# Optimization experiments

Hardware: AMD Instinct MI355X
Metric: run time of the kernel (lower is better)

## Reference

```python
import jax, jax.numpy as jnp
import numpy as np

BN_EPS = 1e-5

def _conv1x1(w, b, x):
    # w: (O, C), b: (O,), x: (B, C, T) -> (B, O, T)
    return jnp.einsum('oc,bct->bot', w, x) + b[None, :, None]

def _maxpool2(x):
    # MaxPool1d(kernel_size=2, stride=2): (B, C, T) -> (B, C, T//2)
    B, C, T = x.shape
    return x.reshape(B, C, T // 2, 2).max(axis=-1)

def setup_inputs() -> dict:
    key = jax.random.key(0)
    ks = jax.random.split(key, 11)
    B, C, Ci, T = 4, 256, 128, 8192
    s_in = 1.0 / np.sqrt(C)
    s_ic = 1.0 / np.sqrt(Ci)
    return {
        'x':       jax.random.normal(ks[0], (B, C, T), dtype=jnp.float32),
        'theta_w': jax.random.uniform(ks[1], (Ci, C), jnp.float32, -s_in, s_in),
        'theta_b': jax.random.uniform(ks[2], (Ci,),   jnp.float32, -s_in, s_in),
        'phi_w':   jax.random.uniform(ks[3], (Ci, C), jnp.float32, -s_in, s_in),
        'phi_b':   jax.random.uniform(ks[4], (Ci,),   jnp.float32, -s_in, s_in),
        'g_w':     jax.random.uniform(ks[5], (Ci, C), jnp.float32, -s_in, s_in),
        'g_b':     jax.random.uniform(ks[6], (Ci,),   jnp.float32, -s_in, s_in),
        'w_w':     jax.random.uniform(ks[7], (C, Ci), jnp.float32, -s_ic, s_ic),
        'w_b':     jax.random.uniform(ks[8], (C,),    jnp.float32, -s_ic, s_ic),
        'gamma':   jax.random.normal(ks[9], (C,), dtype=jnp.float32),
        'beta':    jax.random.normal(ks[10], (C,), dtype=jnp.float32),
    }

def reference(x, theta_w, theta_b, phi_w, phi_b, g_w, g_b, w_w, w_b, gamma, beta):
    # x: (B, C, T)
    theta = _conv1x1(theta_w, theta_b, x)            # (B, Ci, T)
    phi   = _maxpool2(_conv1x1(phi_w, phi_b, x))     # (B, Ci, N), N = T//2
    g     = _maxpool2(_conv1x1(g_w, g_b, x))         # (B, Ci, N)
    N = phi.shape[-1]
    # f = theta^T phi / N  (dot-product similarity, divide-by-N normalization)
    f = jnp.einsum('bct,bcn->btn', theta, phi) / N   # (B, T, N)
    y = jnp.einsum('btn,bcn->bct', f, g)             # (B, Ci, T)
    wy = _conv1x1(w_w, w_b, y)                       # (B, C, T)
    # BatchNorm1d (training mode: batch statistics over (B, T), biased var)
    mean = wy.mean(axis=(0, 2), keepdims=True)
    var = ((wy - mean) ** 2).mean(axis=(0, 2), keepdims=True)
    bn = gamma[None, :, None] * (wy - mean) * jax.lax.rsqrt(var + BN_EPS) + beta[None, :, None]
    return bn + x
```

## Files before the change

### kernel.cpp

```cpp
#include <hip/hip_runtime.h>
#include <hip/hip_bf16.h>


constexpr int B = 4, C = 256, CI = 128, T = 8192, NN = 4096;

using s16x8 = __attribute__((ext_vector_type(8))) short;
using f32x4 = __attribute__((ext_vector_type(4))) float;

__device__ __forceinline__ unsigned short f2bf(float f) {
    unsigned int x = __float_as_uint(f);
    unsigned int r = (x + 0x7fffu + ((x >> 16) & 1u)) >> 16;
    return (unsigned short)r;
}
__device__ __forceinline__ float bf2f(unsigned short u) {
    return __uint_as_float((unsigned int)u << 16);
}

#define MFMA(a, b, c) __builtin_amdgcn_mfma_f32_16x16x32_bf16((a), (b), (c), 0, 0, 0)

__device__ __forceinline__ void glds16(const unsigned short* g, void* l) {
    __builtin_amdgcn_global_load_lds(
        (const __attribute__((address_space(1))) unsigned int*)(g),
        (__attribute__((address_space(3))) unsigned int*)(l), 16, 0, 0);
}


constexpr size_t SZ_XT = (size_t)B * T * C * 2;
constexpr size_t O_XTH = 0;
constexpr size_t O_XTL = O_XTH + SZ_XT;
constexpr size_t O_WSH = O_XTL + SZ_XT;
constexpr size_t O_WSL = O_WSH + (size_t)C * C * 2;
constexpr size_t SZ_P  = (size_t)B * CI * NN * 2;
constexpr size_t O_PH  = O_WSL + (size_t)C * C * 2;
constexpr size_t O_PL  = O_PH + SZ_P;
constexpr size_t O_GH  = O_PL + SZ_P;
constexpr size_t O_GL  = O_GH + SZ_P;
constexpr size_t O_WY  = O_PH;
constexpr size_t O_S   = O_GL + SZ_P;
constexpr size_t O_M   = O_S  + (size_t)B * CI * CI * 4;
constexpr size_t O_W2H = O_M  + (size_t)B * C * CI * 4;
constexpr size_t O_W2L = O_W2H + (size_t)B * C * C * 2;
constexpr size_t O_B2  = O_W2L + (size_t)B * C * C * 2;
constexpr size_t O_GS  = O_B2 + (size_t)B * C * 4;
constexpr size_t O_GQ  = O_GS + (size_t)C * 4;
constexpr size_t O_A   = O_GQ + (size_t)C * 4;
constexpr size_t O_SH  = O_A  + (size_t)C * 4;

__global__ __launch_bounds__(256) void k0_split(
    const float* __restrict__ x, unsigned short* __restrict__ xth,
    unsigned short* __restrict__ xtl)
{
    __shared__ float xs[64][65];
    int t0 = blockIdx.x * 64, c0 = blockIdx.y * 64, b = blockIdx.z;
    int tid = threadIdx.x;
    const float* xb = x + (size_t)b * C * T;
    #pragma unroll
    for (int p = 0; p < 4; ++p) {
        int idx = tid + p * 256;
        int cr = idx >> 4;
        int tg = (idx & 15) * 4;
        float4 v = *reinterpret_cast<const float4*>(xb + (size_t)(c0 + cr) * T + t0 + tg);
        xs[tg + 0][cr] = v.x; xs[tg + 1][cr] = v.y;
        xs[tg + 2][cr] = v.z; xs[tg + 3][cr] = v.w;
    }
    __syncthreads();
    size_t tileBase = ((size_t)b * (T / 128) + (t0 >> 7)) * 32768;
    int trBase = t0 & 127;
    #pragma unroll
    for (int p = 0; p < 2; ++p) {
        int idx = tid + p * 256;
        int kcL = idx >> 6;
        int tl  = idx & 63;
        s16x8 hs, ls;
        #pragma unroll
        for (int j = 0; j < 8; ++j) {
            float v = xs[tl][kcL * 8 + j];
            unsigned short h = f2bf(v);
            unsigned short l = f2bf(v - bf2f(h));
            hs[j] = (short)h; ls[j] = (short)l;
        }
        size_t dst = tileBase + (size_t)((c0 >> 3) + kcL) * 1024 + (trBase + tl) * 8;
        *reinterpret_cast<s16x8*>(xth + dst) = hs;
        *reinterpret_cast<s16x8*>(xtl + dst) = ls;
    }
}

__global__ __launch_bounds__(256) void k0w(
    const float* __restrict__ phi_w, const float* __restrict__ g_w,
    unsigned short* __restrict__ wsh, unsigned short* __restrict__ wsl)
{
    int idx = blockIdx.x * 256 + threadIdx.x;
    int c8 = idx & 31, row = idx >> 5;
    const float* src = (row < CI) ? &phi_w[(size_t)row * C + c8 * 8]
                                  : &g_w[(size_t)(row - CI) * C + c8 * 8];
    s16x8 hs, ls;
    #pragma unroll
    for (int j = 0; j < 8; ++j) {
        float v = src[j];
        unsigned short h = f2bf(v);
        hs[j] = (short)h; ls[j] = (short)f2bf(v - bf2f(h));
    }
    size_t dst = (size_t)(row >> 7) * 32768 + (size_t)c8 * 1024 + (row & 127) * 8;
    *reinterpret_cast<s16x8*>(wsh + dst) = hs;
    *reinterpret_cast<s16x8*>(wsl + dst) = ls;
}

#define STAGE_A(srcT) {                                                        \
    _Pragma("unroll")                                                          \
    for (int i_ = 0; i_ < 16; ++i_)                                            \
        glds16((srcT) + (size_t)(w * 8192 + i_ * 512 + lane * 8),              \
               arena + w * 16384 + i_ * 1024);                                 \
}

#define K8(BT) {                                                               \
    _Pragma("unroll")                                                          \
    for (int ks_ = 0; ks_ < 8; ++ks_) {                                        \
        s16x8 af[4], bfr[4];                                                   \
        _Pragma("unroll")                                                      \
        for (int ts_ = 0; ts_ < 4; ++ts_)                                      \
            af[ts_] = *(const s16x8*)(arena + (ks_ * 4 + lk) * 2048            \
                                      + (wt * 64 + ts_ * 16 + lr) * 16);       \
        _Pragma("unroll")                                                      \
        for (int os_ = 0; os_ < 4; ++os_)                                      \
            bfr[os_] = *(const s16x8*)((BT) + (size_t)(ks_ * 4 + lk) * 1024    \
                                       + (wo * 64 + os_ * 16 + lr) * 8);       \
        _Pragma("unroll")                                                      \
        for (int os_ = 0; os_ < 4; ++os_)                                      \
            _Pragma("unroll")                                                  \
            for (int ts_ = 0; ts_ < 4; ++ts_)                                  \
                acc[os_][ts_] = MFMA(af[ts_], bfr[os_], acc[os_][ts_]);        \
    }                                                                          \
}

#define GEMM_3PHASE(aT_h, aT_l, bT_h, bT_l) {                                  \
    STAGE_A(aT_h);                                                             \
    __syncthreads();                                                           \
    K8(bT_h);                                                                  \
    K8(bT_l);                                                                  \
    __syncthreads();                                                           \
    STAGE_A(aT_l);                                                             \
    __syncthreads();                                                           \
    K8(bT_h);                                                                  \
}

__global__ __launch_bounds__(256, 2) void k1_mfma(
    const unsigned short* __restrict__ xth, const unsigned short* __restrict__ xtl,
    const unsigned short* __restrict__ wsh, const unsigned short* __restrict__ wsl,
    const float* __restrict__ phi_b, const float* __restrict__ g_b,
    unsigned short* __restrict__ ph, unsigned short* __restrict__ pl,
    unsigned short* __restrict__ gh, unsigned short* __restrict__ gl)
{
    const int b = blockIdx.z, t0 = blockIdx.x * 128, isG = blockIdx.y;
    __shared__ __align__(16) char arena[65536];
    const int tid = threadIdx.x, lane = tid & 63, w = tid >> 6;
    const int lr = lane & 15, lk = lane >> 4;
    const int wt = w >> 1, wo = w & 1;

    const unsigned short* aTh = xth + ((size_t)b * (T / 128) + (t0 >> 7)) * 32768;
    const unsigned short* aTl = xtl + ((size_t)b * (T / 128) + (t0 >> 7)) * 32768;
    const unsigned short* bTh = wsh + (size_t)isG * 32768;
    const unsigned short* bTl = wsl + (size_t)isG * 32768;

    f32x4 acc[4][4];
    #pragma unroll
    for (int i = 0; i < 4; ++i)
        #pragma unroll
        for (int j = 0; j < 4; ++j) acc[i][j] = (f32x4){0.f, 0.f, 0.f, 0.f};

    GEMM_3PHASE(aTh, aTl, bTh, bTl)
    __syncthreads();

    unsigned int (*pool_s)[65] = (unsigned int (*)[65])arena;
    const float* biasArr = isG ? g_b : phi_b;
    #pragma unroll
    for (int os = 0; os < 4; ++os) {
        int oL = wo * 64 + os * 16 + lr;
        float bias = biasArr[oL];
        #pragma unroll
        for (int ts = 0; ts < 4; ++ts) {
            f32x4 v = acc[os][ts];
            float m0 = fmaxf(v[0], v[1]) + bias;
            float m1 = fmaxf(v[2], v[3]) + bias;
            int nl = wt * 32 + ts * 8 + lk * 2;
            unsigned short h0 = f2bf(m0), h1 = f2bf(m1);
            pool_s[oL][nl]     = (unsigned int)h0 | ((unsigned int)f2bf(m0 - bf2f(h0)) << 16);
            pool_s[oL][nl + 1] = (unsigned int)h1 | ((unsigned int)f2bf(m1 - bf2f(h1)) << 16);
        }
    }
    __syncthreads();
    int oL = tid >> 1, seg = tid & 1;
    size_t n0 = (size_t)(t0 >> 1) + seg * 32;
    unsigned short* dh = (isG ? gh : ph) + ((size_t)b * CI + oL) * NN + n0;
    unsigned short* dl = (isG ? gl : pl) + ((size_t)b * CI + oL) * NN + n0;
    #pragma unroll
    for (int g4 = 0; g4 < 4; ++g4) {
        s16x8 hs, ls;
        #pragma unroll
        for (int j = 0; j < 8; ++j) {
            unsigned int u = pool_s[oL][seg * 32 + g4 * 8 + j];
            hs[j] = (short)(u & 0xffffu);
            ls[j] = (short)(u >> 16);
        }
        *reinterpret_cast<s16x8*>(dh + g4 * 8) = hs;
        *reinterpret_cast<s16x8*>(dl + g4 * 8) = ls;
    }
}

__global__ __launch_bounds__(256, 2) void k45_stats(
    const unsigned short* __restrict__ xth, const unsigned short* __restrict__ xtl,
    const unsigned short* __restrict__ w2h, const unsigned short* __restrict__ w2l,
    const float* __restrict__ b2, unsigned short* __restrict__ wy,
    float* __restrict__ gsum, float* __restrict__ gsq)
{
    const int b = blockIdx.z, t0 = blockIdx.x * 128, oHalf = blockIdx.y;
    const int o0 = oHalf * 128;
    __shared__ __align__(16) char arena[65536];
    const int tid = threadIdx.x, lane = tid & 63, w = tid >> 6;
    const int lr = lane & 15, lk = lane >> 4;
    const int wt = w >> 1, wo = w & 1;

    const unsigned short* aTh = xth + ((size_t)b * (T / 128) + (t0 >> 7)) * 32768;
    const unsigned short* aTl = xtl + ((size_t)b * (T / 128) + (t0 >> 7)) * 32768;
    const unsigned short* bTh = w2h + ((size_t)b * 2 + oHalf) * 32768;
    const unsigned short* bTl = w2l + ((size_t)b * 2 + oHalf) * 32768;

    f32x4 acc[4][4];
    #pragma unroll
    for (int i = 0; i < 4; ++i)
        #pragma unroll
        for (int j = 0; j < 4; ++j) acc[i][j] = (f32x4){0.f, 0.f, 0.f, 0.f};

    GEMM_3PHASE(aTh, aTl, bTh, bTl)

    #pragma unroll
    for (int os = 0; os < 4; ++os) {
        int o = o0 + wo * 64 + os * 16 + lr;
        float bv = b2[(size_t)b * C + o];
        float s = 0.f, q = 0.f;
        #pragma unroll
        for (int ts = 0; ts < 4; ++ts) {
            int t = t0 + wt * 64 + ts * 16 + lk * 4;
            ushort4 pk;
            float v0 = acc[os][ts][0] + bv;
            float v1 = acc[os][ts][1] + bv;
            float v2 = acc[os][ts][2] + bv;
            float v3 = acc[os][ts][3] + bv;
            s += v0 + v1 + v2 + v3;
            q += v0 * v0 + v1 * v1 + v2 * v2 + v3 * v3;
            pk.x = f2bf(v0); pk.y = f2bf(v1); pk.z = f2bf(v2); pk.w = f2bf(v3);
            *reinterpret_cast<ushort4*>(&wy[((size_t)b * C + o) * T + t]) = pk;
        }
        s += __shfl_xor(s, 16); s += __shfl_xor(s, 32);
        q += __shfl_xor(q, 16); q += __shfl_xor(q, 32);
        if (lk == 0) { atomicAdd(&gsum[o], s); atomicAdd(&gsq[o], q); }
    }
}

__global__ void k4b_stats(const float* __restrict__ gsum, const float* __restrict__ gsq,
                          const float* __restrict__ gamma, const float* __restrict__ beta,
                          float* __restrict__ a, float* __restrict__ sh)
{
    int c = threadIdx.x;
    const float invBT = 1.f / (float)(B * T);
    float mean = gsum[c] * invBT;
    float var  = gsq[c] * invBT - mean * mean;
    float av = gamma[c] * rsqrtf(var + 1e-5f);
    a[c]  = av;
    sh[c] = beta[c] - av * mean;
}

__global__ __launch_bounds__(256) void k5_apply(
    const float* __restrict__ x, const unsigned short* __restrict__ wy,
    const float* __restrict__ a, const float* __restrict__ sh,
    float* __restrict__ out)
{
    size_t total4 = (size_t)B * C * T / 4;
    for (size_t i = (size_t)blockIdx.x * blockDim.x + threadIdx.x; i < total4;
         i += (size_t)gridDim.x * blockDim.x) {
        size_t e = i * 4;
        int c = (int)((e / T) % C);
        ushort4 w4 = *reinterpret_cast<const ushort4*>(&wy[e]);
        float4 x4 = reinterpret_cast<const float4*>(x)[i];
        float av = a[c], sv = sh[c];
        float4 o;
        o.x = av * bf2f(w4.x) + sv + x4.x;
        o.y = av * bf2f(w4.y) + sv + x4.y;
        o.z = av * bf2f(w4.z) + sv + x4.z;
        o.w = av * bf2f(w4.w) + sv + x4.w;
        reinterpret_cast<float4*>(out)[i] = o;
    }
}

__global__ __launch_bounds__(256, 2) void k2_mfma(
    const unsigned short* __restrict__ ph, const unsigned short* __restrict__ pl,
    const unsigned short* __restrict__ gh, const unsigned short* __restrict__ gl,
    float* __restrict__ S)
{
    int b = blockIdx.y, n0 = blockIdx.x * 128;
    int tid = threadIdx.x, lane = tid & 63, w = tid >> 6;
    int lr = lane & 15, lk = lane >> 4;

    f32x4 acc[2][8];
    #pragma unroll
    for (int i = 0; i < 2; ++i)
        #pragma unroll
        for (int j = 0; j < 8; ++j) acc[i][j] = (f32x4){0.f, 0.f, 0.f, 0.f};

    const unsigned short* ah_b = gh + ((size_t)b * CI + w * 32 + lr) * NN + n0 + lk * 8;
    const unsigned short* al_b = gl + ((size_t)b * CI + w * 32 + lr) * NN + n0 + lk * 8;
    const unsigned short* bh_b = ph + ((size_t)b * CI + lr) * NN + n0 + lk * 8;
    const unsigned short* bl_b = pl + ((size_t)b * CI + lr) * NN + n0 + lk * 8;

    for (int ks = 0; ks < 4; ++ks) {
        s16x8 Ah[2], Al[2], Bh[8], Bl[8];
        #pragma unroll
        for (int is = 0; is < 2; ++is) {
            Ah[is] = *reinterpret_cast<const s16x8*>(ah_b + (size_t)is * 16 * NN + ks * 32);
            Al[is] = *reinterpret_cast<const s16x8*>(al_b + (size_t)is * 16 * NN + ks * 32);
        }
        #pragma unroll
        for (int js = 0; js < 8; ++js) {
            Bh[js] = *reinterpret_cast<const s16x8*>(bh_b + (size_t)js * 16 * NN + ks * 32);
            Bl[js] = *reinterpret_cast<const s16x8*>(bl_b + (size_t)js * 16 * NN + ks * 32);
        }
        #pragma unroll
        for (int is = 0; is < 2; ++is)
            #pragma unroll
            for (int js = 0; js < 8; ++js) {
                acc[is][js] = MFMA(Ah[is], Bh[js], acc[is][js]);
                acc[is][js] = MFMA(Al[is], Bh[js], acc[is][js]);
                acc[is][js] = MFMA(Ah[is], Bl[js], acc[is][js]);
            }
    }
    #pragma unroll
    for (int is = 0; is < 2; ++is) {
        int i0 = w * 32 + is * 16 + lk * 4;
        #pragma unroll
        for (int js = 0; js < 8; ++js) {
            int j = js * 16 + lr;
            #pragma unroll
            for (int r = 0; r < 4; ++r)
                atomicAdd(&S[((size_t)b * CI + i0 + r) * CI + j], acc[is][js][r]);
        }
    }
}

__global__ __launch_bounds__(256) void k3a_M(
    const float* __restrict__ w_w, const float* __restrict__ S, float* __restrict__ M)
{
    int idx = blockIdx.x * 256 + threadIdx.x;
    int j4 = (idx & 31) * 4;
    int r  = (idx >> 5) & (C - 1);
    int b  = idx >> 13;
    const float* Sb = S + (size_t)b * CI * CI;
    const float* wr = w_w + (size_t)r * CI;
    float4 a = {0.f, 0.f, 0.f, 0.f};
    for (int k = 0; k < CI; ++k) {
        float wv = wr[k];
        float4 s = *reinterpret_cast<const float4*>(&Sb[(size_t)k * CI + j4]);
        a.x += wv * s.x; a.y += wv * s.y; a.z += wv * s.z; a.w += wv * s.w;
    }
    const float sc = 1.f / NN;
    a.x *= sc; a.y *= sc; a.z *= sc; a.w *= sc;
    *reinterpret_cast<float4*>(&M[((size_t)b * C + r) * CI + j4]) = a;
}

__global__ __launch_bounds__(256) void k3b_W2(
    const float* __restrict__ M, const float* __restrict__ theta_w,
    const float* __restrict__ theta_b, const float* __restrict__ w_b,
    unsigned short* __restrict__ w2h, unsigned short* __restrict__ w2l,
    float* __restrict__ b2)
{
    int idx = blockIdx.x * 256 + threadIdx.x;
    int c8 = idx & 31;
    int r  = (idx >> 5) & (C - 1);
    int b  = idx >> 13;
    const float* Mb = M + ((size_t)b * C + r) * CI;
    float4 a0 = {0.f, 0.f, 0.f, 0.f}, a1 = {0.f, 0.f, 0.f, 0.f};
    for (int k = 0; k < CI; ++k) {
        float mv = Mb[k];
        const float* tw = &theta_w[(size_t)k * C + c8 * 8];
        float4 t0 = *reinterpret_cast<const float4*>(tw);
        float4 t1 = *reinterpret_cast<const float4*>(tw + 4);
        a0.x += mv * t0.x; a0.y += mv * t0.y; a0.z += mv * t0.z; a0.w += mv * t0.w;
        a1.x += mv * t1.x; a1.y += mv * t1.y; a1.z += mv * t1.z; a1.w += mv * t1.w;
    }
    float av[8] = {a0.x, a0.y, a0.z, a0.w, a1.x, a1.y, a1.z, a1.w};
    s16x8 hs, ls;
    #pragma unroll
    for (int i = 0; i < 8; ++i) {
        unsigned short h = f2bf(av[i]);
        hs[i] = (short)h; ls[i] = (short)f2bf(av[i] - bf2f(h));
    }
    size_t dst = ((size_t)b * 2 + (r >> 7)) * 32768 + (size_t)c8 * 1024 + (r & 127) * 8;
    *reinterpret_cast<s16x8*>(w2h + dst) = hs;
    *reinterpret_cast<s16x8*>(w2l + dst) = ls;
    if (c8 == 0) {
        float bv = 0.f;
        for (int k = 0; k < CI; ++k) bv += Mb[k] * theta_b[k];
        b2[(size_t)b * C + r] = bv + w_b[r];
    }
}

extern "C" void kernel_launch(void* const* d_in, const int* in_sizes, int n_in,
                              void* d_out, int out_size, void* d_ws, size_t ws_size,
                              hipStream_t stream)
{
    const float* x       = (const float*)d_in[0];
    const float* theta_w = (const float*)d_in[1];
    const float* theta_b = (const float*)d_in[2];
    const float* phi_w   = (const float*)d_in[3];
    const float* phi_b   = (const float*)d_in[4];
    const float* g_w     = (const float*)d_in[5];
    const float* g_b     = (const float*)d_in[6];
    const float* w_w     = (const float*)d_in[7];
    const float* w_b     = (const float*)d_in[8];
    const float* gamma   = (const float*)d_in[9];
    const float* beta    = (const float*)d_in[10];
    float* out = (float*)d_out;
    char* ws = (char*)d_ws;

    unsigned short* xth = (unsigned short*)(ws + O_XTH);
    unsigned short* xtl = (unsigned short*)(ws + O_XTL);
    unsigned short* wsh = (unsigned short*)(ws + O_WSH);
    unsigned short* wsl = (unsigned short*)(ws + O_WSL);
    unsigned short* ph  = (unsigned short*)(ws + O_PH);
    unsigned short* pl  = (unsigned short*)(ws + O_PL);
    unsigned short* gh  = (unsigned short*)(ws + O_GH);
    unsigned short* gl  = (unsigned short*)(ws + O_GL);
    unsigned short* wy  = (unsigned short*)(ws + O_WY);
    float* Sbuf  = (float*)(ws + O_S);
    float* Mbuf  = (float*)(ws + O_M);
    unsigned short* w2h = (unsigned short*)(ws + O_W2H);
    unsigned short* w2l = (unsigned short*)(ws + O_W2L);
    float* b2    = (float*)(ws + O_B2);
    float* gsum  = (float*)(ws + O_GS);
    float* gsq   = (float*)(ws + O_GQ);
    float* abuf  = (float*)(ws + O_A);
    float* shbuf = (float*)(ws + O_SH);

    hipMemsetAsync(Sbuf, 0, (size_t)B * CI * CI * sizeof(float), stream);
    hipMemsetAsync(gsum, 0, 2 * (size_t)C * sizeof(float), stream);

    k0_split<<<dim3(T / 64, C / 64, B), 256, 0, stream>>>(x, xth, xtl);
    k0w<<<dim3(32), 256, 0, stream>>>(phi_w, g_w, wsh, wsl);
    k1_mfma<<<dim3(T / 128, 2, B), 256, 0, stream>>>(xth, xtl, wsh, wsl, phi_b, g_b,
                                                     ph, pl, gh, gl);
    k2_mfma<<<dim3(NN / 128, B), 256, 0, stream>>>(ph, pl, gh, gl, Sbuf);
    k3a_M<<<dim3(B * C * CI / 4 / 256), 256, 0, stream>>>(w_w, Sbuf, Mbuf);
    k3b_W2<<<dim3(B * C * C / 8 / 256), 256, 0, stream>>>(Mbuf, theta_w, theta_b, w_b,
                                                          w2h, w2l, b2);
    k45_stats<<<dim3(T / 128, C / 128, B), 256, 0, stream>>>(
        xth, xtl, w2h, w2l, b2, wy, gsum, gsq);
    k4b_stats<<<1, C, 0, stream>>>(gsum, gsq, gamma, beta, abuf, shbuf);
    k5_apply<<<2048, 256, 0, stream>>>(x, wy, abuf, shbuf, out);
}
```

Measured before the change: 243.6 us.

## Double-buffer A and B tiles in LDS across 24 k-steps in GEMM kernels

Replaces the three-phase GEMM, which staged a whole 64KB A tile and read B straight from global memory, with a 24-step loop. Each step stages one small A and B chunk (hi/lo split terms) into a double-buffered 32KB LDS arena, prefetching the next chunk while computing on the current one. This reduces LDS use so launch bounds can rise to 4 blocks per CU, aiming to hide global load latency and raise occupancy. The cost is a __syncthreads on every k-step, and the tighter register budget at the higher occupancy may cause spilling.

```diff
diff --git a/kernel.cpp b/kernel.cpp
--- a/kernel.cpp
+++ b/kernel.cpp
@@ -105,45 +105,44 @@
     *reinterpret_cast<s16x8*>(wsl + dst) = ls;
 }
 
-#define STAGE_A(srcT) {                                                        \
+#define STAGE_(buf, ks) {                                                      \
+    const int r_ = (ks) >> 3, c_ = (ks) & 7;                                   \
+    const unsigned short* As_ = (r_ == 2) ? aTl : aTh;                         \
+    const unsigned short* Bs_ = (r_ == 1) ? bTl : bTh;                         \
+    size_t so_ = (size_t)c_ * 4096 + (size_t)w * 1024 + (size_t)lane * 8;      \
+    char* da_ = arena + (buf) * 16384 + w * 2048;                              \
+    glds16(As_ + so_,       da_);                                              \
+    glds16(As_ + so_ + 512, da_ + 1024);                                       \
+    glds16(Bs_ + so_,       da_ + 8192);                                       \
+    glds16(Bs_ + so_ + 512, da_ + 8192 + 1024);                                \
+}
+
+#define GEMM_M97() {                                                           \
+    STAGE_(0, 0);                                                              \
+    __syncthreads();                                                           \
     _Pragma("unroll")                                                          \
-    for (int i_ = 0; i_ < 16; ++i_)                                            \
-        glds16((srcT) + (size_t)(w * 8192 + i_ * 512 + lane * 8),              \
-               arena + w * 16384 + i_ * 1024);                                 \
-}
-
-#define K8(BT) {                                                               \
-    _Pragma("unroll")                                                          \
-    for (int ks_ = 0; ks_ < 8; ++ks_) {                                        \
+    for (int ks = 0; ks < 24; ++ks) {                                          \
+        const int cur = ks & 1;                                                \
+        if (ks + 1 < 24) { STAGE_(cur ^ 1, ks + 1); }                          \
         s16x8 af[4], bfr[4];                                                   \
         _Pragma("unroll")                                                      \
         for (int ts_ = 0; ts_ < 4; ++ts_)                                      \
-            af[ts_] = *(const s16x8*)(arena + (ks_ * 4 + lk) * 2048            \
+            af[ts_] = *(const s16x8*)(arena + cur * 16384 + lk * 2048          \
                                       + (wt * 64 + ts_ * 16 + lr) * 16);       \
         _Pragma("unroll")                                                      \
         for (int os_ = 0; os_ < 4; ++os_)                                      \
-            bfr[os_] = *(const s16x8*)((BT) + (size_t)(ks_ * 4 + lk) * 1024    \
-                                       + (wo * 64 + os_ * 16 + lr) * 8);       \
+            bfr[os_] = *(const s16x8*)(arena + cur * 16384 + 8192 + lk * 2048  \
+                                       + (wo * 64 + os_ * 16 + lr) * 16);      \
         _Pragma("unroll")                                                      \
         for (int os_ = 0; os_ < 4; ++os_)                                      \
             _Pragma("unroll")                                                  \
             for (int ts_ = 0; ts_ < 4; ++ts_)                                  \
                 acc[os_][ts_] = MFMA(af[ts_], bfr[os_], acc[os_][ts_]);        \
+        __syncthreads();                                                       \
     }                                                                          \
 }
 
-#define GEMM_3PHASE(aT_h, aT_l, bT_h, bT_l) {                                  \
-    STAGE_A(aT_h);                                                             \
-    __syncthreads();                                                           \
-    K8(bT_h);                                                                  \
-    K8(bT_l);                                                                  \
-    __syncthreads();                                                           \
-    STAGE_A(aT_l);                                                             \
-    __syncthreads();                                                           \
-    K8(bT_h);                                                                  \
-}
-
-__global__ __launch_bounds__(256, 2) void k1_mfma(
+__global__ __launch_bounds__(256, 4) void k1_mfma(
     const unsigned short* __restrict__ xth, const unsigned short* __restrict__ xtl,
     const unsigned short* __restrict__ wsh, const unsigned short* __restrict__ wsl,
     const float* __restrict__ phi_b, const float* __restrict__ g_b,
@@ -151,7 +150,7 @@
     unsigned short* __restrict__ gh, unsigned short* __restrict__ gl)
 {
     const int b = blockIdx.z, t0 = blockIdx.x * 128, isG = blockIdx.y;
-    __shared__ __align__(16) char arena[65536];
+    __shared__ __align__(16) char arena[33280];
     const int tid = threadIdx.x, lane = tid & 63, w = tid >> 6;
     const int lr = lane & 15, lk = lane >> 4;
     const int wt = w >> 1, wo = w & 1;
@@ -167,7 +166,7 @@
         #pragma unroll
         for (int j = 0; j < 4; ++j) acc[i][j] = (f32x4){0.f, 0.f, 0.f, 0.f};
 
-    GEMM_3PHASE(aTh, aTl, bTh, bTl)
+    GEMM_M97()
     __syncthreads();
 
     unsigned int (*pool_s)[65] = (unsigned int (*)[65])arena;
@@ -206,7 +205,7 @@
     }
 }
 
-__global__ __launch_bounds__(256, 2) void k45_stats(
+__global__ __launch_bounds__(256, 4) void k45_stats(
     const unsigned short* __restrict__ xth, const unsigned short* __restrict__ xtl,
     const unsigned short* __restrict__ w2h, const unsigned short* __restrict__ w2l,
     const float* __restrict__ b2, unsigned short* __restrict__ wy,
@@ -214,7 +213,7 @@
 {
     const int b = blockIdx.z, t0 = blockIdx.x * 128, oHalf = blockIdx.y;
     const int o0 = oHalf * 128;
-    __shared__ __align__(16) char arena[65536];
+    __shared__ __align__(16) char arena[32768];
     const int tid = threadIdx.x, lane = tid & 63, w = tid >> 6;
     const int lr = lane & 15, lk = lane >> 4;
     const int wt = w >> 1, wo = w & 1;
@@ -230,7 +229,7 @@
         #pragma unroll
         for (int j = 0; j < 4; ++j) acc[i][j] = (f32x4){0.f, 0.f, 0.f, 0.f};
 
-    GEMM_3PHASE(aTh, aTl, bTh, bTl)
+    GEMM_M97()
 
     #pragma unroll
     for (int os = 0; os < 4; ++os) {
```

After: 252.8 us. 1.04x slower.
